# Kernel optimization log

Measured on AMD Instinct MI355X. Metric: run time of the kernel, lower is better.

Reference implementation:

```python
import jax, jax.numpy as jnp
import numpy as np

N, T, H, W, C = 64, 32, 64, 64, 256
HID, NB, P, OUT = 512, 12, 7, 388
CIN = P * P + 2  # 49 patch values + 2 normalized coords


def _ln(x, s):
    # haiku LayerNorm(axis=-1, create_scale=True, create_offset=False), eps=1e-5
    m = jnp.mean(x, axis=-1, keepdims=True)
    v = jnp.var(x, axis=-1, keepdims=True)
    return (x - m) * jax.lax.rsqrt(v + 1e-5) * s


def _dwconv(x, w, b, groups):
    # hk.DepthwiseConv1D, NWC, stride 1, SAME padding; w: [K, 1, C_out]
    y = jax.lax.conv_general_dilated(
        x, w, (1,), 'SAME', dimension_numbers=('NWC', 'WIO', 'NWC'),
        feature_group_count=groups)
    return y + b


def _forward(feature_grid, query_feats, pos, in_w, in_b, dw1_w, dw1_b, dw2_w,
             dw2_b, ln1_s, ln2_s, up_w, up_b, down_w, down_b, lnf_s, out_w,
             out_b):
    pad = P - 1
    # cost volume: einsum('bnc,bthwc->tbnhw') with batch=1, laid out [N,T,H,W]
    corrs = jnp.einsum('nc,thwc->nthw', query_feats, feature_grid)
    padded = jnp.pad(corrs, ((0, 0), (0, 0), (pad, pad), (pad, pad)))
    # extract_patch_depthwise_conv: the separable bilinear bump kernel convolved
    # VALID over the padded map equals a bilinear sample at (o + pos + P/2 - 1).
    pp = pos + P / 2.0 - 1.0  # [N,T,2] (y,x)
    iy = jnp.floor(pp[..., 0])
    ix = jnp.floor(pp[..., 1])
    fy = (pp[..., 0] - iy)[..., None, None]
    fx = (pp[..., 1] - ix)[..., None, None]
    offs = jnp.arange(P, dtype=jnp.int32)
    y0 = iy.astype(jnp.int32)[..., None] + offs  # [N,T,P]
    x0 = ix.astype(jnp.int32)[..., None] + offs  # [N,T,P]
    gat = jax.vmap(jax.vmap(lambda img, yi, xi: img[yi][:, xi]))
    patch = ((1 - fy) * (1 - fx) * gat(padded, y0, x0)
             + (1 - fy) * fx * gat(padded, y0, x0 + 1)
             + fy * (1 - fx) * gat(padded, y0 + 1, x0)
             + fy * fx * gat(padded, y0 + 1, x0 + 1))  # [N,T,P,P]
    x = jnp.concatenate(
        [patch.reshape(patch.shape[0], patch.shape[1], P * P),
         pos / jnp.float32(H)], axis=-1)  # [N,T,CIN]
    # PIPSMLPMixer
    x = x @ in_w + in_b  # [N,T,HID]
    for i in range(NB):
        # PIPsConvBlock: depthwise_conv_residual
        skip = x
        h = _ln(x, ln1_s[i])
        h = jax.nn.gelu(_dwconv(h, dw1_w[i], dw1_b[i], HID))  # ch mult 4
        h = _dwconv(h, dw2_w[i], dw2_b[i], HID * 4)           # ch mult 1
        h = h[..., 0::4] + h[..., 1::4] + h[..., 2::4] + h[..., 3::4]
        x = h + skip
        # conv_channels_mixer
        skip = x
        h = _ln(x, ln2_s[i])
        h = jax.nn.gelu(h @ up_w[i] + up_b[i]) @ down_w[i] + down_b[i]
        x = h + skip
    x = _ln(x, lnf_s)
    return x @ out_w + out_b  # [N,T,OUT]


def setup_inputs() -> dict:
    key = jax.random.key(0)
    ks = jax.random.split(key, 12)
    s = 0.02
    return dict(
        feature_grid=jax.random.normal(ks[0], (T, H, W, C), jnp.float32),
        query_feats=jax.random.normal(ks[1], (N, C), jnp.float32),
        pos=jax.random.uniform(ks[2], (N, T, 2), jnp.float32) * (H - 8),
        in_w=jax.random.normal(ks[3], (CIN, HID), jnp.float32) * s,
        in_b=jnp.zeros((HID,), jnp.float32),
        dw1_w=jax.random.normal(ks[4], (NB, 3, 1, HID * 4), jnp.float32) * s,
        dw1_b=jnp.zeros((NB, HID * 4), jnp.float32),
        dw2_w=jax.random.normal(ks[5], (NB, 3, 1, HID * 4), jnp.float32) * s,
        dw2_b=jnp.zeros((NB, HID * 4), jnp.float32),
        ln1_s=jnp.ones((NB, HID), jnp.float32),
        ln2_s=jnp.ones((NB, HID), jnp.float32),
        up_w=jax.random.normal(ks[6], (NB, HID, HID * 4), jnp.float32) * s,
        up_b=jnp.zeros((NB, HID * 4), jnp.float32),
        down_w=jax.random.normal(ks[7], (NB, HID * 4, HID), jnp.float32) * s,
        down_b=jnp.zeros((NB, HID), jnp.float32),
        lnf_s=jnp.ones((HID,), jnp.float32),
        out_w=jax.random.normal(ks[8], (HID, OUT), jnp.float32) * s,
        out_b=jnp.zeros((OUT,), jnp.float32),
    )


def reference(feature_grid, query_feats, pos, in_w, in_b, dw1_w, dw1_b, dw2_w,
              dw2_b, ln1_s, ln2_s, up_w, up_b, down_w, down_b, lnf_s, out_w,
              out_b):
    return _forward(feature_grid, query_feats, pos, in_w, in_b, dw1_w, dw1_b,
                    dw2_w, dw2_b, ln1_s, ln2_s, up_w, up_b, down_w, down_b,
                    lnf_s, out_w, out_b)
```

## Files before the change

### kernel.cpp

```cpp
#include <hip/hip_runtime.h>
#include <hip/hip_bf16.h>

#define N_    64
#define T_    32
#define H_    64
#define W_    64
#define C_    256
#define HID   512
#define HID4  2048
#define NBLK  12
#define P_    7
#define OUT_  388
#define OUTP  448
#define CIN   51
#define M_    (N_*T_)

typedef __attribute__((ext_vector_type(4))) float f32x4;
typedef __attribute__((ext_vector_type(8))) short bf16x8;

__device__ __forceinline__ float gelu_f(float x) {
    float x3 = x * x * x;
    return 0.5f * x * (1.f + tanhf(0.7978845608028654f * (x + 0.044715f * x3)));
}

__device__ __forceinline__ void gload_lds16(const void* g, void* l) {
    __builtin_amdgcn_global_load_lds(
        (const __attribute__((address_space(1))) void*)g,
        (__attribute__((address_space(3))) void*)l, 16, 0, 0);
}

__global__ __launch_bounds__(256) void patch_kernel(
    const float* __restrict__ fg, const float* __restrict__ qf,
    const float* __restrict__ pos, const float* __restrict__ in_w,
    const float* __restrict__ in_b, float* __restrict__ x) {
    __shared__ float4 q[64];
    __shared__ float g[8][8];
    __shared__ float xrow[CIN];
    int m = blockIdx.x;
    int n = m >> 5;
    int t = m & (T_ - 1);
    int tid = threadIdx.x, wid = tid >> 6, lane = tid & 63;
    if (tid < 64) q[tid] = *(const float4*)&qf[n * C_ + tid * 4];
    __syncthreads();
    float posy = pos[m * 2 + 0];
    float posx = pos[m * 2 + 1];
    float py = posy + 2.5f;
    float px = posx + 2.5f;
    int iy = (int)floorf(py), ix = (int)floorf(px);
    float fy = py - (float)iy, fx = px - (float)ix;
    float4 qv = q[lane];
    #pragma unroll
    for (int i = 0; i < 16; ++i) {
        int idx = wid * 16 + i;
        int a = idx >> 3, b = idx & 7;
        int y = iy + a - 6, xc = ix + b - 6;
        float partial = 0.f;
        if (y >= 0 && y < H_ && xc >= 0 && xc < W_) {
            const float4* fp = (const float4*)&fg[(((t * H_ + y) * W_) + xc) * C_];
            float4 v = fp[lane];
            partial = v.x * qv.x + v.y * qv.y + v.z * qv.z + v.w * qv.w;
        }
        #pragma unroll
        for (int o2 = 32; o2; o2 >>= 1) partial += __shfl_xor(partial, o2);
        if (lane == 0) g[a][b] = partial;
    }
    __syncthreads();
    if (tid < 49) {
        int p = tid / 7, qq = tid % 7;
        xrow[tid] = (1.f - fy) * (1.f - fx) * g[p][qq]
                  + (1.f - fy) * fx         * g[p][qq + 1]
                  + fy         * (1.f - fx) * g[p + 1][qq]
                  + fy         * fx         * g[p + 1][qq + 1];
    } else if (tid == 49) {
        xrow[49] = posy * (1.f / 64.f);
    } else if (tid == 50) {
        xrow[50] = posx * (1.f / 64.f);
    }
    __syncthreads();
    float acc0 = in_b[tid], acc1 = in_b[tid + 256];
    #pragma unroll
    for (int c = 0; c < CIN; ++c) {
        float rv = xrow[c];
        acc0 += rv * in_w[c * HID + tid];
        acc1 += rv * in_w[c * HID + tid + 256];
    }
    x[m * HID + tid] = acc0;
    x[m * HID + tid + 256] = acc1;
}

__global__ __launch_bounds__(512) void fused_dw_kernel(
    const float* __restrict__ xin, float* __restrict__ xout,
    __hip_bfloat16* __restrict__ t1T,
    const float* __restrict__ ln1s, const float* __restrict__ ln2s,
    const float* __restrict__ w1, const float* __restrict__ b1,
    const float* __restrict__ w2, const float* __restrict__ b2) {
    __shared__ float2 part[12][8];
    int n = blockIdx.y;
    int t0 = blockIdx.x * 8;
    int j = threadIdx.x;
    int lane = j & 63, wave = j >> 6;

    float xv[12];
    #pragma unroll
    for (int tt = 0; tt < 12; ++tt) {
        int t = t0 - 2 + tt;
        xv[tt] = (t >= 0 && t < T_) ? xin[(n * T_ + t) * HID + j] : 0.f;
    }
    #pragma unroll
    for (int tt = 0; tt < 12; ++tt) {
        float s = xv[tt], q = xv[tt] * xv[tt];
        #pragma unroll
        for (int o = 32; o; o >>= 1) { s += __shfl_xor(s, o); q += __shfl_xor(q, o); }
        if (lane == 0) part[tt][wave] = make_float2(s, q);
    }
    __syncthreads();
    float s1v = ln1s[j];
    float xl[12];
    #pragma unroll
    for (int tt = 0; tt < 12; ++tt) {
        int t = t0 - 2 + tt;
        if (t >= 0 && t < T_) {
            float s = 0.f, q = 0.f;
            #pragma unroll
            for (int w = 0; w < 8; ++w) { float2 p = part[tt][w]; s += p.x; q += p.y; }
            float mean = s * (1.f / HID);
            float var  = q * (1.f / HID) - mean * mean;
            xl[tt] = (xv[tt] - mean) * rsqrtf(var + 1e-5f) * s1v;
        } else xl[tt] = 0.f;
    }
    float w1a[12], w2a[12], b1a[4];
    #pragma unroll
    for (int r = 0; r < 3; ++r) {
        *(float4*)&w1a[r * 4] = *(const float4*)&w1[r * HID4 + 4 * j];
        *(float4*)&w2a[r * 4] = *(const float4*)&w2[r * HID4 + 4 * j];
    }
    *(float4*)&b1a[0] = *(const float4*)&b1[4 * j];
    float4 b2v = *(const float4*)&b2[4 * j];
    float h[8];
    float b2sum = b2v.x + b2v.y + b2v.z + b2v.w;
    #pragma unroll
    for (int i = 0; i < 8; ++i) h[i] = b2sum;
    #pragma unroll
    for (int k = 0; k < 4; ++k) {
        float gk[10];
        #pragma unroll
        for (int idx = 0; idx < 10; ++idx) {
            int tp = t0 - 1 + idx;
            if (tp >= 0 && tp < T_) {
                float a = b1a[k] + w1a[0 * 4 + k] * xl[idx]
                                 + w1a[1 * 4 + k] * xl[idx + 1]
                                 + w1a[2 * 4 + k] * xl[idx + 2];
                gk[idx] = gelu_f(a);
            } else gk[idx] = 0.f;
        }
        #pragma unroll
        for (int i = 0; i < 8; ++i)
            h[i] += w2a[0 * 4 + k] * gk[i] + w2a[1 * 4 + k] * gk[i + 1]
                  + w2a[2 * 4 + k] * gk[i + 2];
    }
    float xn[8];
    #pragma unroll
    for (int i = 0; i < 8; ++i) xn[i] = xv[i + 2] + h[i];
    __syncthreads();
    #pragma unroll
    for (int i = 0; i < 8; ++i) {
        float s = xn[i], q = xn[i] * xn[i];
        #pragma unroll
        for (int o = 32; o; o >>= 1) { s += __shfl_xor(s, o); q += __shfl_xor(q, o); }
        if (lane == 0) part[i][wave] = make_float2(s, q);
    }
    __syncthreads();
    float s2v = ln2s[j];
    int cbase = j >> 3, csub = j & 7;
    #pragma unroll
    for (int i = 0; i < 8; ++i) {
        float s = 0.f, q = 0.f;
        #pragma unroll
        for (int w = 0; w < 8; ++w) { float2 p = part[i][w]; s += p.x; q += p.y; }
        float mean = s * (1.f / HID);
        float var  = q * (1.f / HID) - mean * mean;
        float rstd = rsqrtf(var + 1e-5f);
        int row = n * T_ + t0 + i;
        xout[row * HID + j] = xn[i];
        t1T[((size_t)cbase * M_ + row) * 8 + csub] =
            __float2bfloat16((xn[i] - mean) * rstd * s2v);
    }
}

__global__ __launch_bounds__(256) void ln_kernel(
    const float* __restrict__ in, const float* __restrict__ s,
    __hip_bfloat16* __restrict__ t1T) {
    int wid = threadIdx.x >> 6, lane = threadIdx.x & 63;
    int row = blockIdx.x * 4 + wid;
    const float* r = in + row * HID + lane * 8;
    float4 v0 = *(const float4*)r;
    float4 v1 = *(const float4*)(r + 4);
    float sum = v0.x + v0.y + v0.z + v0.w + v1.x + v1.y + v1.z + v1.w;
    float sq  = v0.x*v0.x + v0.y*v0.y + v0.z*v0.z + v0.w*v0.w
              + v1.x*v1.x + v1.y*v1.y + v1.z*v1.z + v1.w*v1.w;
    #pragma unroll
    for (int o = 32; o; o >>= 1) { sum += __shfl_xor(sum, o); sq += __shfl_xor(sq, o); }
    float mean = sum * (1.f / HID);
    float var  = sq * (1.f / HID) - mean * mean;
    float rstd = rsqrtf(var + 1e-5f);
    const float* sp = s + lane * 8;
    float4 s0 = *(const float4*)sp;
    float4 s1 = *(const float4*)(sp + 4);
    float o[8];
    o[0] = (v0.x - mean) * rstd * s0.x; o[1] = (v0.y - mean) * rstd * s0.y;
    o[2] = (v0.z - mean) * rstd * s0.z; o[3] = (v0.w - mean) * rstd * s0.w;
    o[4] = (v1.x - mean) * rstd * s1.x; o[5] = (v1.y - mean) * rstd * s1.y;
    o[6] = (v1.z - mean) * rstd * s1.z; o[7] = (v1.w - mean) * rstd * s1.w;
    alignas(16) __hip_bfloat16 tmp[8];
    #pragma unroll
    for (int i = 0; i < 8; ++i) tmp[i] = __float2bfloat16(o[i]);
    *(bf16x8*)&t1T[((size_t)lane * M_ + row) * 8] = *(bf16x8*)tmp;
}

__global__ __launch_bounds__(256) void tcvt_kernel(
    const float* __restrict__ src, __hip_bfloat16* __restrict__ dst,
    int R, int C, int Cpad) {
    __shared__ float tile[32][33];
    size_t zb = blockIdx.z;
    src += zb * (size_t)R * C;
    dst += zb * (size_t)Cpad * R;
    int c0 = blockIdx.x * 32, r0 = blockIdx.y * 32;
    int tx = threadIdx.x & 31, ty = threadIdx.x >> 5;
    #pragma unroll
    for (int i = 0; i < 4; ++i) {
        int r = r0 + ty + i * 8, c = c0 + tx;
        tile[ty + i * 8][tx] = (c < C) ? src[(size_t)r * C + c] : 0.f;
    }
    __syncthreads();
    #pragma unroll
    for (int i = 0; i < 4; ++i) {
        int c = c0 + ty + i * 8, r = r0 + tx;
        dst[(size_t)c * R + r] = __float2bfloat16(tile[tx][ty + i * 8]);
    }
}

template <int EPI, int SWZ>
__global__ __launch_bounds__(256, 4) void gemm_regA(
    const __hip_bfloat16* __restrict__ At,
    const __hip_bfloat16* __restrict__ Bt,
    const float* __restrict__ bias, float* __restrict__ Cf,
    __hip_bfloat16* __restrict__ Cb, int ldN, int Nstore) {
    constexpr int K = 512;
    __shared__ alignas(16) __hip_bfloat16 Bs[2][64 * 64];
    int tid = threadIdx.x;
    int lane = tid & 63, w = tid >> 6;

    int row0, col0;
    if (SWZ) {
        int bid = blockIdx.y * gridDim.x + blockIdx.x;
        int chunk = gridDim.y >> 3;
        int xcd = bid & 7;
        int i = bid >> 3;
        row0 = (xcd * chunk + (i % chunk)) * 64;
        col0 = (i / chunk) * 64;
    } else {
        row0 = blockIdx.y * 64;
        col0 = blockIdx.x * 64;
    }

    int sub = lane >> 4;
    int arow = row0 + w * 16 + (lane & 15);
    bf16x8 areg[16];
    #pragma unroll
    for (int kb = 0; kb < 16; ++kb) {
        int c = kb * 4 + sub;
        areg[kb] = *(const bf16x8*)&At[((size_t)c * M_ + arow) * 8];
    }

    int rI = lane >> 3;
    int cp = lane & 7;
    auto stageB = [&](int buf, int k0) {
        #pragma unroll
        for (int s = 0; s < 2; ++s) {
            int rbase = w * 16 + s * 8;
            int row = rbase + rI;
            int corig = cp ^ (row & 7);
            gload_lds16(Bt + (size_t)(col0 + row) * K + k0 + corig * 8,
                        (char*)Bs[buf] + rbase * 128);
        }
    };

    f32x4 acc[4];
    #pragma unroll
    for (int n = 0; n < 4; ++n) acc[n] = (f32x4){0.f, 0.f, 0.f, 0.f};

    stageB(0, 0);
    #pragma unroll
    for (int step = 0; step < 8; ++step) {
        int cur = step & 1;
        __builtin_amdgcn_s_barrier();
        if (step < 7) {
            stageB(cur ^ 1, (step + 1) * 64);
            asm volatile("s_waitcnt vmcnt(2)" ::: "memory");
        } else {
            asm volatile("s_waitcnt vmcnt(0)" ::: "memory");
        }
        __builtin_amdgcn_sched_barrier(0);
        __builtin_amdgcn_s_barrier();
        __builtin_amdgcn_sched_barrier(0);
        #pragma unroll
        for (int kk = 0; kk < 2; ++kk) {
            bf16x8 bfr[4];
            #pragma unroll
            for (int n = 0; n < 4; ++n) {
                int row = n * 16 + (lane & 15);
                int chunk = (kk * 4 + sub) ^ (row & 7);
                bfr[n] = *(const bf16x8*)((const char*)Bs[cur] + row * 128 + chunk * 16);
            }
            __builtin_amdgcn_s_setprio(1);
            #pragma unroll
            for (int n = 0; n < 4; ++n)
                acc[n] = __builtin_amdgcn_mfma_f32_16x16x32_bf16(
                    areg[step * 2 + kk], bfr[n], acc[n], 0, 0, 0);
            __builtin_amdgcn_s_setprio(0);
        }
    }

    int cr = (lane >> 4) * 4;
    int cc = lane & 15;
    #pragma unroll
    for (int n = 0; n < 4; ++n) {
        #pragma unroll
        for (int j = 0; j < 4; ++j) {
            int row = row0 + w * 16 + cr + j;
            int col = col0 + n * 16 + cc;
            float v = acc[n][j];
            if (EPI == 0) {
                if (col < Nstore)
                    Cf[(size_t)row * Nstore + col] = v + bias[col];
            } else {
                v = gelu_f(v + bias[col]);
                Cb[(size_t)row * ldN + col] = __float2bfloat16(v);
            }
        }
    }
}

__global__ __launch_bounds__(512) void gemm_down(
    const __hip_bfloat16* __restrict__ A, const __hip_bfloat16* __restrict__ Bt,
    const float* __restrict__ bias, float* __restrict__ Cf,
    int K, int ldN) {
    __shared__ alignas(16) __hip_bfloat16 As[2][2][64 * 64];
    __shared__ alignas(16) __hip_bfloat16 Bs[2][2][64 * 64];
    int tid = threadIdx.x;
    int lane = tid & 63, wave = tid >> 6;
    int g = wave >> 2;
    int w4 = wave & 3;
    int wr = w4 >> 1, wc = w4 & 1;

    int bid = blockIdx.y * gridDim.x + blockIdx.x;
    int chunk = gridDim.y >> 3;
    int xcd = bid & 7;
    int i = bid >> 3;
    int row0 = (xcd * chunk + (i % chunk)) * 64;
    int col0 = (i / chunk) * 64;

    int Kg = K / 2;
    int kbase = g * Kg;

    f32x4 acc[2][2];
    #pragma unroll
    for (int m = 0; m < 2; ++m)
        #pragma unroll
        for (int n = 0; n < 2; ++n)
            acc[m][n] = (f32x4){0.f, 0.f, 0.f, 0.f};

    int rI = lane >> 3;
    int cp = lane & 7;

    auto stage = [&](int buf, int k0) {
        #pragma unroll
        for (int s = 0; s < 2; ++s) {
            int rbase = w4 * 16 + s * 8;
            int row = rbase + rI;
            int corig = cp ^ (row & 7);
            gload_lds16(A + (size_t)(row0 + row) * K + kbase + k0 + corig * 8,
                        (char*)As[g][buf] + rbase * 128);
        }
        #pragma unroll
        for (int s = 0; s < 2; ++s) {
            int rbase = w4 * 16 + s * 8;
            int row = rbase + rI;
            int corig = cp ^ (row & 7);
            gload_lds16(Bt + (size_t)(col0 + row) * K + kbase + k0 + corig * 8,
                        (char*)Bs[g][buf] + rbase * 128);
        }
    };

    int nsteps = Kg >> 6;
    stage(0, 0);
    for (int step = 0; step < nsteps; ++step) {
        int cur = step & 1;
        __builtin_amdgcn_s_barrier();
        if (step + 1 < nsteps) {
            stage(cur ^ 1, (step + 1) * 64);
            asm volatile("s_waitcnt vmcnt(4)" ::: "memory");
        } else {
            asm volatile("s_waitcnt vmcnt(0)" ::: "memory");
        }
        __builtin_amdgcn_sched_barrier(0);
        __builtin_amdgcn_s_barrier();
        __builtin_amdgcn_sched_barrier(0);
        #pragma unroll
        for (int kk = 0; kk < 2; ++kk) {
            bf16x8 af[2], bfr[2];
            #pragma unroll
            for (int m = 0; m < 2; ++m) {
                int row = wr * 32 + m * 16 + (lane & 15);
                int chunk2 = (kk * 4 + (lane >> 4)) ^ (row & 7);
                af[m] = *(const bf16x8*)((const char*)As[g][cur] + row * 128 + chunk2 * 16);
            }
            #pragma unroll
            for (int n = 0; n < 2; ++n) {
                int row = wc * 32 + n * 16 + (lane & 15);
                int chunk2 = (kk * 4 + (lane >> 4)) ^ (row & 7);
                bfr[n] = *(const bf16x8*)((const char*)Bs[g][cur] + row * 128 + chunk2 * 16);
            }
            __builtin_amdgcn_s_setprio(1);
            #pragma unroll
            for (int m = 0; m < 2; ++m)
                #pragma unroll
                for (int n = 0; n < 2; ++n)
                    acc[m][n] = __builtin_amdgcn_mfma_f32_16x16x32_bf16(
                        af[m], bfr[n], acc[m][n], 0, 0, 0);
            __builtin_amdgcn_s_setprio(0);
        }
    }

    int cr = (lane >> 4) * 4;
    int cc = lane & 15;

    float* scratch = (float*)&As[0][0][0];
    __syncthreads();
    if (g == 1) {
        #pragma unroll
        for (int m = 0; m < 2; ++m)
            #pragma unroll
            for (int n = 0; n < 2; ++n)
                #pragma unroll
                for (int j = 0; j < 4; ++j)
                    scratch[(wr * 32 + m * 16 + cr + j) * 64 +
                            wc * 32 + n * 16 + cc] = acc[m][n][j];
    }
    __syncthreads();
    if (g == 1) return;
    #pragma unroll
    for (int m = 0; m < 2; ++m) {
        #pragma unroll
        for (int n = 0; n < 2; ++n) {
            #pragma unroll
            for (int j = 0; j < 4; ++j) {
                int row = row0 + wr * 32 + m * 16 + cr + j;
                int col = col0 + wc * 32 + n * 16 + cc;
                float v = acc[m][n][j] +
                          scratch[(wr * 32 + m * 16 + cr + j) * 64 +
                                  wc * 32 + n * 16 + cc];
                Cf[(size_t)row * ldN + col] += v + bias[col];
            }
        }
    }
}

extern "C" void kernel_launch(void* const* d_in, const int* in_sizes, int n_in,
                              void* d_out, int out_size, void* d_ws, size_t ws_size,
                              hipStream_t stream) {
    const float* fg     = (const float*)d_in[0];
    const float* qf     = (const float*)d_in[1];
    const float* pos    = (const float*)d_in[2];
    const float* in_w   = (const float*)d_in[3];
    const float* in_b   = (const float*)d_in[4];
    const float* dw1_w  = (const float*)d_in[5];
    const float* dw1_b  = (const float*)d_in[6];
    const float* dw2_w  = (const float*)d_in[7];
    const float* dw2_b  = (const float*)d_in[8];
    const float* ln1_s  = (const float*)d_in[9];
    const float* ln2_s  = (const float*)d_in[10];
    const float* up_w   = (const float*)d_in[11];
    const float* up_b   = (const float*)d_in[12];
    const float* down_w = (const float*)d_in[13];
    const float* down_b = (const float*)d_in[14];
    const float* lnf_s  = (const float*)d_in[15];
    const float* out_w  = (const float*)d_in[16];
    const float* out_b  = (const float*)d_in[17];
    float* out = (float*)d_out;

    char* ws = (char*)d_ws;
    float* xa = (float*)ws;                        ws += (size_t)M_ * HID * 4;
    float* xb = (float*)ws;                        ws += (size_t)M_ * HID * 4;
    __hip_bfloat16* t1T = (__hip_bfloat16*)ws;     ws += (size_t)M_ * HID * 2;
    __hip_bfloat16* t2b = (__hip_bfloat16*)ws;     ws += (size_t)M_ * HID4 * 2;
    __hip_bfloat16* upT  = (__hip_bfloat16*)ws;    ws += (size_t)NBLK * HID4 * HID * 2;
    __hip_bfloat16* dnT  = (__hip_bfloat16*)ws;    ws += (size_t)NBLK * HID * HID4 * 2;
    __hip_bfloat16* outT = (__hip_bfloat16*)ws;    ws += (size_t)OUTP * HID * 2;

    tcvt_kernel<<<dim3(HID4 / 32, HID / 32, NBLK), 256, 0, stream>>>(
        up_w, upT, HID, HID4, HID4);
    tcvt_kernel<<<dim3(HID / 32, HID4 / 32, NBLK), 256, 0, stream>>>(
        down_w, dnT, HID4, HID, HID);
    tcvt_kernel<<<dim3(OUTP / 32, HID / 32, 1), 256, 0, stream>>>(
        out_w, outT, HID, OUT_, OUTP);

    patch_kernel<<<M_, 256, 0, stream>>>(fg, qf, pos, in_w, in_b, xa);

    float* xc = xa;
    float* xn = xb;
    for (int b = 0; b < NBLK; ++b) {
        fused_dw_kernel<<<dim3(4, N_), 512, 0, stream>>>(
            xc, xn, t1T, ln1_s + b * HID, ln2_s + b * HID,
            dw1_w + b * 3 * HID4, dw1_b + b * HID4,
            dw2_w + b * 3 * HID4, dw2_b + b * HID4);
        gemm_regA<1, 1><<<dim3(HID4 / 64, M_ / 64), 256, 0, stream>>>(
            t1T, upT + (size_t)b * HID4 * HID, up_b + b * HID4, nullptr, t2b,
            HID4, HID4);
        gemm_down<<<dim3(HID / 64, M_ / 64), 512, 0, stream>>>(
            t2b, dnT + (size_t)b * HID * HID4, down_b + b * HID, xn,
            HID4, HID);
        float* tmp = xc; xc = xn; xn = tmp;
    }

    ln_kernel<<<M_ / 4, 256, 0, stream>>>(xc, lnf_s, t1T);
    gemm_regA<0, 0><<<dim3(OUTP / 64, M_ / 64), 256, 0, stream>>>(
        t1T, outT, out_b, out, nullptr, OUT_, OUT_);
}
```

Before: 607.3 us.

## Merge weight transposes into patch kernel and reuse A registers across two column tiles

The three weight-transpose launches are folded into the patch kernel as extra blocks, so there is one prologue launch instead of four. The up-projection GEMM now has each block cover two 64-column tiles in sequence while keeping the A fragment in registers. This halves the A reloads and the grid size. The swizzle is hardcoded to 4 row tiles per XCD, which matches M=2048, and the fewer blocks may lower occupancy and latency hiding.

New measurement: 625.1 us. 2.9% more time.

```diff
diff --git a/kernel.cpp b/kernel.cpp
--- a/kernel.cpp
+++ b/kernel.cpp
@@ -29,63 +29,107 @@
         (__attribute__((address_space(3))) void*)l, 16, 0, 0);
 }
 
-__global__ __launch_bounds__(256) void patch_kernel(
+__global__ __launch_bounds__(256) void pre_kernel(
     const float* __restrict__ fg, const float* __restrict__ qf,
     const float* __restrict__ pos, const float* __restrict__ in_w,
-    const float* __restrict__ in_b, float* __restrict__ x) {
+    const float* __restrict__ in_b, float* __restrict__ x,
+    const float* __restrict__ up_w, const float* __restrict__ dn_w,
+    const float* __restrict__ out_w, __hip_bfloat16* __restrict__ upT,
+    __hip_bfloat16* __restrict__ dnT, __hip_bfloat16* __restrict__ outT) {
     __shared__ float4 q[64];
     __shared__ float g[8][8];
     __shared__ float xrow[CIN];
-    int m = blockIdx.x;
-    int n = m >> 5;
-    int t = m & (T_ - 1);
-    int tid = threadIdx.x, wid = tid >> 6, lane = tid & 63;
-    if (tid < 64) q[tid] = *(const float4*)&qf[n * C_ + tid * 4];
+    __shared__ float tile[32][33];
+    int bid = blockIdx.x;
+    int tid = threadIdx.x;
+
+    if (bid < M_) {
+        int m = bid;
+        int n = m >> 5;
+        int t = m & (T_ - 1);
+        int wid = tid >> 6, lane = tid & 63;
+        if (tid < 64) q[tid] = *(const float4*)&qf[n * C_ + tid * 4];
+        __syncthreads();
+        float posy = pos[m * 2 + 0];
+        float posx = pos[m * 2 + 1];
+        float py = posy + 2.5f;
+        float px = posx + 2.5f;
+        int iy = (int)floorf(py), ix = (int)floorf(px);
+        float fy = py - (float)iy, fx = px - (float)ix;
+        float4 qv = q[lane];
+        #pragma unroll
+        for (int i = 0; i < 16; ++i) {
+            int idx = wid * 16 + i;
+            int a = idx >> 3, b = idx & 7;
+            int y = iy + a - 6, xc = ix + b - 6;
+            float partial = 0.f;
+            if (y >= 0 && y < H_ && xc >= 0 && xc < W_) {
+                const float4* fp = (const float4*)&fg[(((t * H_ + y) * W_) + xc) * C_];
+                float4 v = fp[lane];
+                partial = v.x * qv.x + v.y * qv.y + v.z * qv.z + v.w * qv.w;
+            }
+            #pragma unroll
+            for (int o2 = 32; o2; o2 >>= 1) partial += __shfl_xor(partial, o2);
+            if (lane == 0) g[a][b] = partial;
+        }
+        __syncthreads();
+        if (tid < 49) {
+            int p = tid / 7, qq = tid % 7;
+            xrow[tid] = (1.f - fy) * (1.f - fx) * g[p][qq]
+                      + (1.f - fy) * fx         * g[p][qq + 1]
+                      + fy         * (1.f - fx) * g[p + 1][qq]
+                      + fy         * fx         * g[p + 1][qq + 1];
+        } else if (tid == 49) {
+            xrow[49] = posy * (1.f / 64.f);
+        } else if (tid == 50) {
+            xrow[50] = posx * (1.f / 64.f);
+        }
+        __syncthreads();
+        float acc0 = in_b[tid], acc1 = in_b[tid + 256];
+        #pragma unroll
+        for (int c = 0; c < CIN; ++c) {
+            float rv = xrow[c];
+            acc0 += rv * in_w[c * HID + tid];
+            acc1 += rv * in_w[c * HID + tid + 256];
+        }
+        x[m * HID + tid] = acc0;
+        x[m * HID + tid + 256] = acc1;
+        return;
+    }
+
+    bid -= M_;
+    const float* src;
+    __hip_bfloat16* dst;
+    int R, C, bx, by;
+    if (bid < 12288) {
+        int z = bid >> 10, r = bid & 1023;
+        src = up_w + (size_t)z * HID * HID4;
+        dst = upT + (size_t)z * HID4 * HID;
+        R = HID; C = HID4; bx = r & 63; by = r >> 6;
+    } else if (bid < 24576) {
+        bid -= 12288;
+        int z = bid >> 10, r = bid & 1023;
+        src = dn_w + (size_t)z * HID4 * HID;
+        dst = dnT + (size_t)z * HID * HID4;
+        R = HID4; C = HID; bx = r & 15; by = r >> 4;
+    } else {
+        bid -= 24576;
+        src = out_w; dst = outT;
+        R = HID; C = OUT_; bx = bid % 14; by = bid / 14;
+    }
+    int c0 = bx * 32, r0 = by * 32;
+    int tx = tid & 31, ty = tid >> 5;
+    #pragma unroll
+    for (int i = 0; i < 4; ++i) {
+        int r = r0 + ty + i * 8, c = c0 + tx;
+        tile[ty + i * 8][tx] = (c < C) ? src[(size_t)r * C + c] : 0.f;
+    }
     __syncthreads();
-    float posy = pos[m * 2 + 0];
-    float posx = pos[m * 2 + 1];
-    float py = posy + 2.5f;
-    float px = posx + 2.5f;
-    int iy = (int)floorf(py), ix = (int)floorf(px);
-    float fy = py - (float)iy, fx = px - (float)ix;
-    float4 qv = q[lane];
-    #pragma unroll
-    for (int i = 0; i < 16; ++i) {
-        int idx = wid * 16 + i;
-        int a = idx >> 3, b = idx & 7;
-        int y = iy + a - 6, xc = ix + b - 6;
-        float partial = 0.f;
-        if (y >= 0 && y < H_ && xc >= 0 && xc < W_) {
-            const float4* fp = (const float4*)&fg[(((t * H_ + y) * W_) + xc) * C_];
-            float4 v = fp[lane];
-            partial = v.x * qv.x + v.y * qv.y + v.z * qv.z + v.w * qv.w;
-        }
-        #pragma unroll
-        for (int o2 = 32; o2; o2 >>= 1) partial += __shfl_xor(partial, o2);
-        if (lane == 0) g[a][b] = partial;
-    }
-    __syncthreads();
-    if (tid < 49) {
-        int p = tid / 7, qq = tid % 7;
-        xrow[tid] = (1.f - fy) * (1.f - fx) * g[p][qq]
-                  + (1.f - fy) * fx         * g[p][qq + 1]
-                  + fy         * (1.f - fx) * g[p + 1][qq]
-                  + fy         * fx         * g[p + 1][qq + 1];
-    } else if (tid == 49) {
-        xrow[49] = posy * (1.f / 64.f);
-    } else if (tid == 50) {
-        xrow[50] = posx * (1.f / 64.f);
-    }
-    __syncthreads();
-    float acc0 = in_b[tid], acc1 = in_b[tid + 256];
-    #pragma unroll
-    for (int c = 0; c < CIN; ++c) {
-        float rv = xrow[c];
-        acc0 += rv * in_w[c * HID + tid];
-        acc1 += rv * in_w[c * HID + tid + 256];
-    }
-    x[m * HID + tid] = acc0;
-    x[m * HID + tid + 256] = acc1;
+    #pragma unroll
+    for (int i = 0; i < 4; ++i) {
+        int c = c0 + ty + i * 8, r = r0 + tx;
+        dst[(size_t)c * R + r] = __float2bfloat16(tile[tx][ty + i * 8]);
+    }
 }
 
 __global__ __launch_bounds__(512) void fused_dw_kernel(
@@ -217,29 +261,7 @@
     *(bf16x8*)&t1T[((size_t)lane * M_ + row) * 8] = *(bf16x8*)tmp;
 }
 
-__global__ __launch_bounds__(256) void tcvt_kernel(
-    const float* __restrict__ src, __hip_bfloat16* __restrict__ dst,
-    int R, int C, int Cpad) {
-    __shared__ float tile[32][33];
-    size_t zb = blockIdx.z;
-    src += zb * (size_t)R * C;
-    dst += zb * (size_t)Cpad * R;
-    int c0 = blockIdx.x * 32, r0 = blockIdx.y * 32;
-    int tx = threadIdx.x & 31, ty = threadIdx.x >> 5;
-    #pragma unroll
-    for (int i = 0; i < 4; ++i) {
-        int r = r0 + ty + i * 8, c = c0 + tx;
-        tile[ty + i * 8][tx] = (c < C) ? src[(size_t)r * C + c] : 0.f;
-    }
-    __syncthreads();
-    #pragma unroll
-    for (int i = 0; i < 4; ++i) {
-        int c = c0 + ty + i * 8, r = r0 + tx;
-        dst[(size_t)c * R + r] = __float2bfloat16(tile[tx][ty + i * 8]);
-    }
-}
-
-template <int EPI, int SWZ>
+template <int EPI, int SWZ, int NT>
 __global__ __launch_bounds__(256, 4) void gemm_regA(
     const __hip_bfloat16* __restrict__ At,
     const __hip_bfloat16* __restrict__ Bt,
@@ -250,17 +272,16 @@
     int tid = threadIdx.x;
     int lane = tid & 63, w = tid >> 6;
 
-    int row0, col0;
+    int row0, col0base;
     if (SWZ) {
         int bid = blockIdx.y * gridDim.x + blockIdx.x;
-        int chunk = gridDim.y >> 3;
         int xcd = bid & 7;
         int i = bid >> 3;
-        row0 = (xcd * chunk + (i % chunk)) * 64;
-        col0 = (i / chunk) * 64;
+        row0 = (xcd * 4 + (i & 3)) * 64;
+        col0base = (i >> 2) * (64 * NT);
     } else {
         row0 = blockIdx.y * 64;
-        col0 = blockIdx.x * 64;
+        col0base = blockIdx.x * (64 * NT);
     }
 
     int sub = lane >> 4;
@@ -274,7 +295,7 @@
 
     int rI = lane >> 3;
     int cp = lane & 7;
-    auto stageB = [&](int buf, int k0) {
+    auto stageB = [&](int buf, int k0, int col0) {
         #pragma unroll
         for (int s = 0; s < 2; ++s) {
             int rbase = w * 16 + s * 8;
@@ -285,57 +306,62 @@
         }
     };
 
-    f32x4 acc[4];
-    #pragma unroll
-    for (int n = 0; n < 4; ++n) acc[n] = (f32x4){0.f, 0.f, 0.f, 0.f};
-
-    stageB(0, 0);
-    #pragma unroll
-    for (int step = 0; step < 8; ++step) {
-        int cur = step & 1;
-        __builtin_amdgcn_s_barrier();
-        if (step < 7) {
-            stageB(cur ^ 1, (step + 1) * 64);
-            asm volatile("s_waitcnt vmcnt(2)" ::: "memory");
-        } else {
-            asm volatile("s_waitcnt vmcnt(0)" ::: "memory");
-        }
-        __builtin_amdgcn_sched_barrier(0);
-        __builtin_amdgcn_s_barrier();
-        __builtin_amdgcn_sched_barrier(0);
-        #pragma unroll
-        for (int kk = 0; kk < 2; ++kk) {
-            bf16x8 bfr[4];
-            #pragma unroll
-            for (int n = 0; n < 4; ++n) {
-                int row = n * 16 + (lane & 15);
-                int chunk = (kk * 4 + sub) ^ (row & 7);
-                bfr[n] = *(const bf16x8*)((const char*)Bs[cur] + row * 128 + chunk * 16);
-            }
-            __builtin_amdgcn_s_setprio(1);
-            #pragma unroll
-            for (int n = 0; n < 4; ++n)
-                acc[n] = __builtin_amdgcn_mfma_f32_16x16x32_bf16(
-                    areg[step * 2 + kk], bfr[n], acc[n], 0, 0, 0);
-            __builtin_amdgcn_s_setprio(0);
-        }
-    }
-
     int cr = (lane >> 4) * 4;
     int cc = lane & 15;
-    #pragma unroll
-    for (int n = 0; n < 4; ++n) {
-        #pragma unroll
-        for (int j = 0; j < 4; ++j) {
-            int row = row0 + w * 16 + cr + j;
-            int col = col0 + n * 16 + cc;
-            float v = acc[n][j];
-            if (EPI == 0) {
-                if (col < Nstore)
-                    Cf[(size_t)row * Nstore + col] = v + bias[col];
+
+    #pragma unroll 1
+    for (int t = 0; t < NT; ++t) {
+        int col0 = col0base + t * 64;
+        f32x4 acc[4];
+        #pragma unroll
+        for (int n = 0; n < 4; ++n) acc[n] = (f32x4){0.f, 0.f, 0.f, 0.f};
+
+        stageB(0, 0, col0);
+        #pragma unroll
+        for (int step = 0; step < 8; ++step) {
+            int cur = step & 1;
+            __builtin_amdgcn_s_barrier();
+            if (step < 7) {
+                stageB(cur ^ 1, (step + 1) * 64, col0);
+                asm volatile("s_waitcnt vmcnt(2)" ::: "memory");
             } else {
-                v = gelu_f(v + bias[col]);
-                Cb[(size_t)row * ldN + col] = __float2bfloat16(v);
+                asm volatile("s_waitcnt vmcnt(0)" ::: "memory");
+            }
+            __builtin_amdgcn_sched_barrier(0);
+            __builtin_amdgcn_s_barrier();
+            __builtin_amdgcn_sched_barrier(0);
+            #pragma unroll
+            for (int kk = 0; kk < 2; ++kk) {
+                bf16x8 bfr[4];
+                #pragma unroll
+                for (int n = 0; n < 4; ++n) {
+                    int row = n * 16 + (lane & 15);
+                    int chunk = (kk * 4 + sub) ^ (row & 7);
+                    bfr[n] = *(const bf16x8*)((const char*)Bs[cur] + row * 128 + chunk * 16);
+                }
+                __builtin_amdgcn_s_setprio(1);
+                #pragma unroll
+                for (int n = 0; n < 4; ++n)
+                    acc[n] = __builtin_amdgcn_mfma_f32_16x16x32_bf16(
+                        areg[step * 2 + kk], bfr[n], acc[n], 0, 0, 0);
+                __builtin_amdgcn_s_setprio(0);
+            }
+        }
+
+        #pragma unroll
+        for (int n = 0; n < 4; ++n) {
+            #pragma unroll
+            for (int j = 0; j < 4; ++j) {
+                int row = row0 + w * 16 + cr + j;
+                int col = col0 + n * 16 + cc;
+                float v = acc[n][j];
+                if (EPI == 0) {
+                    if (col < Nstore)
+                        Cf[(size_t)row * Nstore + col] = v + bias[col];
+                } else {
+                    v = gelu_f(v + bias[col]);
+                    Cb[(size_t)row * ldN + col] = __float2bfloat16(v);
+                }
             }
         }
     }
@@ -354,11 +380,10 @@
     int wr = w4 >> 1, wc = w4 & 1;
 
     int bid = blockIdx.y * gridDim.x + blockIdx.x;
-    int chunk = gridDim.y >> 3;
     int xcd = bid & 7;
     int i = bid >> 3;
-    int row0 = (xcd * chunk + (i % chunk)) * 64;
-    int col0 = (i / chunk) * 64;
+    int row0 = (xcd * 4 + (i & 3)) * 64;
+    int col0 = (i >> 2) * 64;
 
     int Kg = K / 2;
     int kbase = g * Kg;
@@ -498,14 +523,8 @@
     __hip_bfloat16* dnT  = (__hip_bfloat16*)ws;    ws += (size_t)NBLK * HID * HID4 * 2;
     __hip_bfloat16* outT = (__hip_bfloat16*)ws;    ws += (size_t)OUTP * HID * 2;
 
-    tcvt_kernel<<<dim3(HID4 / 32, HID / 32, NBLK), 256, 0, stream>>>(
-        up_w, upT, HID, HID4, HID4);
-    tcvt_kernel<<<dim3(HID / 32, HID4 / 32, NBLK), 256, 0, stream>>>(
-        down_w, dnT, HID4, HID, HID);
-    tcvt_kernel<<<dim3(OUTP / 32, HID / 32, 1), 256, 0, stream>>>(
-        out_w, outT, HID, OUT_, OUTP);
-
-    patch_kernel<<<M_, 256, 0, stream>>>(fg, qf, pos, in_w, in_b, xa);
+    pre_kernel<<<26848, 256, 0, stream>>>(
+        fg, qf, pos, in_w, in_b, xa, up_w, down_w, out_w, upT, dnT, outT);
 
     float* xc = xa;
     float* xn = xb;
@@ -514,7 +533,7 @@
             xc, xn, t1T, ln1_s + b * HID, ln2_s + b * HID,
             dw1_w + b * 3 * HID4, dw1_b + b * HID4,
             dw2_w + b * 3 * HID4, dw2_b + b * HID4);
-        gemm_regA<1, 1><<<dim3(HID4 / 64, M_ / 64), 256, 0, stream>>>(
+        gemm_regA<1, 1, 2><<<dim3(HID4 / 128, M_ / 64), 256, 0, stream>>>(
             t1T, upT + (size_t)b * HID4 * HID, up_b + b * HID4, nullptr, t2b,
             HID4, HID4);
         gemm_down<<<dim3(HID / 64, M_ / 64), 512, 0, stream>>>(
@@ -524,6 +543,6 @@
     }
 
     ln_kernel<<<M_ / 4, 256, 0, stream>>>(xc, lnf_s, t1T);
-    gemm_regA<0, 0><<<dim3(OUTP / 64, M_ / 64), 256, 0, stream>>>(
+    gemm_regA<0, 0, 1><<<dim3(OUTP / 64, M_ / 64), 256, 0, stream>>>(
         t1T, outT, out_b, out, nullptr, OUT_, OUT_);
 }
```

## Overlap per-block weight transpose-convert with down GEMM via extra blocks

Applied to the files above, without the earlier changes.

Removes the three up-front bulk weight transpose/convert kernels. Block 0's weights and out_w are now converted by a single combined kernel, and each later block's up/down weights are converted by 256 extra workgroups appended to the previous block's down-projection GEMM launch. This spreads the one-time conversion across the layer loop so it can fill idle CUs during the small down GEMM. The GEMM tile swizzles are hardcoded for the fixed grid shape, and gemm_down's shared memory becomes a union with the transpose tile. The tradeoff is a larger down-GEMM grid and a shared-memory footprint that could limit occupancy.

Result: no change. 614.1 us (+1.1%).

```diff
diff --git a/kernel.cpp b/kernel.cpp
--- a/kernel.cpp
+++ b/kernel.cpp
@@ -29,6 +29,39 @@
         (__attribute__((address_space(3))) void*)l, 16, 0, 0);
 }
 
+__device__ __forceinline__ void tcvt_tile(
+    const float* __restrict__ src, __hip_bfloat16* __restrict__ dst,
+    int R, int C, int r0, int c0, int tid, float (*tile)[65]) {
+    int rrb = tid >> 4;
+    int c4 = (tid & 15) * 4;
+    #pragma unroll
+    for (int i = 0; i < 4; ++i) {
+        int rr = rrb + i * 32;
+        int c = c0 + c4;
+        float4 v;
+        if (c + 3 < C) {
+            v = *(const float4*)&src[(size_t)(r0 + rr) * C + c];
+        } else {
+            v.x = (c + 0 < C) ? src[(size_t)(r0 + rr) * C + c + 0] : 0.f;
+            v.y = (c + 1 < C) ? src[(size_t)(r0 + rr) * C + c + 1] : 0.f;
+            v.z = (c + 2 < C) ? src[(size_t)(r0 + rr) * C + c + 2] : 0.f;
+            v.w = (c + 3 < C) ? src[(size_t)(r0 + rr) * C + c + 3] : 0.f;
+        }
+        tile[rr][c4 + 0] = v.x;
+        tile[rr][c4 + 1] = v.y;
+        tile[rr][c4 + 2] = v.z;
+        tile[rr][c4 + 3] = v.w;
+    }
+    __syncthreads();
+    int rr = tid & 127;
+    int ch = tid >> 7;
+    #pragma unroll
+    for (int i = 0; i < 16; ++i) {
+        int cc = ch + i * 4;
+        dst[(size_t)(c0 + cc) * R + r0 + rr] = __float2bfloat16(tile[rr][cc]);
+    }
+}
+
 __global__ __launch_bounds__(256) void patch_kernel(
     const float* __restrict__ fg, const float* __restrict__ qf,
     const float* __restrict__ pos, const float* __restrict__ in_w,
@@ -86,6 +119,24 @@
     }
     x[m * HID + tid] = acc0;
     x[m * HID + tid + 256] = acc1;
+}
+
+__global__ __launch_bounds__(512) void tcvt0_kernel(
+    const float* __restrict__ up_w, const float* __restrict__ dn_w,
+    const float* __restrict__ out_w, __hip_bfloat16* __restrict__ upT,
+    __hip_bfloat16* __restrict__ dnT, __hip_bfloat16* __restrict__ outT) {
+    __shared__ float tile[128][65];
+    int bid = blockIdx.x;
+    int tid = threadIdx.x;
+    if (bid < 128) {
+        tcvt_tile(up_w, upT, HID, HID4, (bid >> 5) * 128, (bid & 31) * 64, tid, tile);
+    } else if (bid < 256) {
+        bid -= 128;
+        tcvt_tile(dn_w, dnT, HID4, HID, (bid >> 3) * 128, (bid & 7) * 64, tid, tile);
+    } else {
+        bid -= 256;
+        tcvt_tile(out_w, outT, HID, OUT_, (bid / 7) * 128, (bid % 7) * 64, tid, tile);
+    }
 }
 
 __global__ __launch_bounds__(512) void fused_dw_kernel(
@@ -217,28 +268,6 @@
     *(bf16x8*)&t1T[((size_t)lane * M_ + row) * 8] = *(bf16x8*)tmp;
 }
 
-__global__ __launch_bounds__(256) void tcvt_kernel(
-    const float* __restrict__ src, __hip_bfloat16* __restrict__ dst,
-    int R, int C, int Cpad) {
-    __shared__ float tile[32][33];
-    size_t zb = blockIdx.z;
-    src += zb * (size_t)R * C;
-    dst += zb * (size_t)Cpad * R;
-    int c0 = blockIdx.x * 32, r0 = blockIdx.y * 32;
-    int tx = threadIdx.x & 31, ty = threadIdx.x >> 5;
-    #pragma unroll
-    for (int i = 0; i < 4; ++i) {
-        int r = r0 + ty + i * 8, c = c0 + tx;
-        tile[ty + i * 8][tx] = (c < C) ? src[(size_t)r * C + c] : 0.f;
-    }
-    __syncthreads();
-    #pragma unroll
-    for (int i = 0; i < 4; ++i) {
-        int c = c0 + ty + i * 8, r = r0 + tx;
-        dst[(size_t)c * R + r] = __float2bfloat16(tile[tx][ty + i * 8]);
-    }
-}
-
 template <int EPI, int SWZ>
 __global__ __launch_bounds__(256, 4) void gemm_regA(
     const __hip_bfloat16* __restrict__ At,
@@ -253,11 +282,10 @@
     int row0, col0;
     if (SWZ) {
         int bid = blockIdx.y * gridDim.x + blockIdx.x;
-        int chunk = gridDim.y >> 3;
         int xcd = bid & 7;
         int i = bid >> 3;
-        row0 = (xcd * chunk + (i % chunk)) * 64;
-        col0 = (i / chunk) * 64;
+        row0 = (xcd * 4 + (i & 3)) * 64;
+        col0 = (i >> 2) * 64;
     } else {
         row0 = blockIdx.y * 64;
         col0 = blockIdx.x * 64;
@@ -341,24 +369,44 @@
     }
 }
 
+union DnSmem {
+    struct { __hip_bfloat16 As[2][2][64 * 64]; __hip_bfloat16 Bs[2][2][64 * 64]; } g;
+    float tile[128][65];
+};
+
 __global__ __launch_bounds__(512) void gemm_down(
     const __hip_bfloat16* __restrict__ A, const __hip_bfloat16* __restrict__ Bt,
     const float* __restrict__ bias, float* __restrict__ Cf,
+    const float* __restrict__ up_w_n, const float* __restrict__ dn_w_n,
+    __hip_bfloat16* __restrict__ upT_n, __hip_bfloat16* __restrict__ dnT_n,
     int K, int ldN) {
-    __shared__ alignas(16) __hip_bfloat16 As[2][2][64 * 64];
-    __shared__ alignas(16) __hip_bfloat16 Bs[2][2][64 * 64];
+    __shared__ DnSmem sm;
     int tid = threadIdx.x;
+    int bid = blockIdx.x;
+
+    if (bid >= 256) {
+        if (up_w_n == nullptr) return;
+        int b2 = bid - 256;
+        if (b2 < 128) {
+            tcvt_tile(up_w_n, upT_n, HID, HID4,
+                      (b2 >> 5) * 128, (b2 & 31) * 64, tid, sm.tile);
+        } else {
+            b2 -= 128;
+            tcvt_tile(dn_w_n, dnT_n, HID4, HID,
+                      (b2 >> 3) * 128, (b2 & 7) * 64, tid, sm.tile);
+        }
+        return;
+    }
+
     int lane = tid & 63, wave = tid >> 6;
     int g = wave >> 2;
     int w4 = wave & 3;
     int wr = w4 >> 1, wc = w4 & 1;
 
-    int bid = blockIdx.y * gridDim.x + blockIdx.x;
-    int chunk = gridDim.y >> 3;
     int xcd = bid & 7;
     int i = bid >> 3;
-    int row0 = (xcd * chunk + (i % chunk)) * 64;
-    int col0 = (i / chunk) * 64;
+    int row0 = (xcd * 4 + (i & 3)) * 64;
+    int col0 = (i >> 2) * 64;
 
     int Kg = K / 2;
     int kbase = g * Kg;
@@ -380,7 +428,7 @@
             int row = rbase + rI;
             int corig = cp ^ (row & 7);
             gload_lds16(A + (size_t)(row0 + row) * K + kbase + k0 + corig * 8,
-                        (char*)As[g][buf] + rbase * 128);
+                        (char*)sm.g.As[g][buf] + rbase * 128);
         }
         #pragma unroll
         for (int s = 0; s < 2; ++s) {
@@ -388,7 +436,7 @@
             int row = rbase + rI;
             int corig = cp ^ (row & 7);
             gload_lds16(Bt + (size_t)(col0 + row) * K + kbase + k0 + corig * 8,
-                        (char*)Bs[g][buf] + rbase * 128);
+                        (char*)sm.g.Bs[g][buf] + rbase * 128);
         }
     };
 
@@ -413,13 +461,15 @@
             for (int m = 0; m < 2; ++m) {
                 int row = wr * 32 + m * 16 + (lane & 15);
                 int chunk2 = (kk * 4 + (lane >> 4)) ^ (row & 7);
-                af[m] = *(const bf16x8*)((const char*)As[g][cur] + row * 128 + chunk2 * 16);
+                af[m] = *(const bf16x8*)((const char*)sm.g.As[g][cur] +
+                                         row * 128 + chunk2 * 16);
             }
             #pragma unroll
             for (int n = 0; n < 2; ++n) {
                 int row = wc * 32 + n * 16 + (lane & 15);
                 int chunk2 = (kk * 4 + (lane >> 4)) ^ (row & 7);
-                bfr[n] = *(const bf16x8*)((const char*)Bs[g][cur] + row * 128 + chunk2 * 16);
+                bfr[n] = *(const bf16x8*)((const char*)sm.g.Bs[g][cur] +
+                                          row * 128 + chunk2 * 16);
             }
             __builtin_amdgcn_s_setprio(1);
             #pragma unroll
@@ -435,7 +485,7 @@
     int cr = (lane >> 4) * 4;
     int cc = lane & 15;
 
-    float* scratch = (float*)&As[0][0][0];
+    float* scratch = (float*)&sm.g.As[0][0][0];
     __syncthreads();
     if (g == 1) {
         #pragma unroll
@@ -498,14 +548,8 @@
     __hip_bfloat16* dnT  = (__hip_bfloat16*)ws;    ws += (size_t)NBLK * HID * HID4 * 2;
     __hip_bfloat16* outT = (__hip_bfloat16*)ws;    ws += (size_t)OUTP * HID * 2;
 
-    tcvt_kernel<<<dim3(HID4 / 32, HID / 32, NBLK), 256, 0, stream>>>(
-        up_w, upT, HID, HID4, HID4);
-    tcvt_kernel<<<dim3(HID / 32, HID4 / 32, NBLK), 256, 0, stream>>>(
-        down_w, dnT, HID4, HID, HID);
-    tcvt_kernel<<<dim3(OUTP / 32, HID / 32, 1), 256, 0, stream>>>(
-        out_w, outT, HID, OUT_, OUTP);
-
     patch_kernel<<<M_, 256, 0, stream>>>(fg, qf, pos, in_w, in_b, xa);
+    tcvt0_kernel<<<284, 512, 0, stream>>>(up_w, down_w, out_w, upT, dnT, outT);
 
     float* xc = xa;
     float* xn = xb;
@@ -517,8 +561,13 @@
         gemm_regA<1, 1><<<dim3(HID4 / 64, M_ / 64), 256, 0, stream>>>(
             t1T, upT + (size_t)b * HID4 * HID, up_b + b * HID4, nullptr, t2b,
             HID4, HID4);
-        gemm_down<<<dim3(HID / 64, M_ / 64), 512, 0, stream>>>(
+        bool last = (b == NBLK - 1);
+        gemm_down<<<512, 512, 0, stream>>>(
             t2b, dnT + (size_t)b * HID * HID4, down_b + b * HID, xn,
+            last ? nullptr : up_w + (size_t)(b + 1) * HID * HID4,
+            last ? nullptr : down_w + (size_t)(b + 1) * HID4 * HID,
+            upT + (size_t)(b + 1) * HID4 * HID,
+            dnT + (size_t)(b + 1) * HID * HID4,
             HID4, HID);
         float* tmp = xc; xc = xn; xn = tmp;
     }
```
